# Optimization experiments

Hardware: AMD Instinct MI355X
Metric: run time of the kernel (lower is better)

Reference implementation:

```python
import jax, jax.numpy as jnp
import numpy as np

B, T, N, D, TXT, TE, H = 8, 8192, 256, 512, 768, 2048, 8
DH = D // H


def _ln(x, g, b):
    m = jnp.mean(x, axis=-1, keepdims=True)
    v = jnp.mean(jnp.square(x - m), axis=-1, keepdims=True)
    return (x - m) * jax.lax.rsqrt(v + 1e-5) * g + b


def setup_inputs() -> dict:
    key = jax.random.key(0)
    ks = jax.random.split(key, 10)
    s = 0.02  # init scale for weights (zero_module init replaced by small random for a non-trivial baseline)
    return {
        "x": jax.random.normal(ks[0], (B, T, D), jnp.float32),
        "xf": jax.random.normal(ks[1], (B, N, TXT), jnp.float32),
        "emb": jax.random.normal(ks[2], (B, TE), jnp.float32),
        "ln_x_g": jnp.ones((D,), jnp.float32),
        "ln_x_b": jnp.zeros((D,), jnp.float32),
        "ln_t_g": jnp.ones((TXT,), jnp.float32),
        "ln_t_b": jnp.zeros((TXT,), jnp.float32),
        "Wq": jax.random.normal(ks[3], (D, D), jnp.float32) * s,
        "bq": jnp.zeros((D,), jnp.float32),
        "Wk": jax.random.normal(ks[4], (TXT, D), jnp.float32) * s,
        "bk": jnp.zeros((D,), jnp.float32),
        "Wv": jax.random.normal(ks[5], (TXT, D), jnp.float32) * s,
        "bv": jnp.zeros((D,), jnp.float32),
        "emb_W": jax.random.normal(ks[6], (TE, 2 * D), jnp.float32) * s,
        "emb_b": jnp.zeros((2 * D,), jnp.float32),
        "ln_o_g": jnp.ones((D,), jnp.float32),
        "ln_o_b": jnp.zeros((D,), jnp.float32),
        "out_W": jax.random.normal(ks[7], (D, D), jnp.float32) * s,
        "out_b": jnp.zeros((D,), jnp.float32),
    }


def reference(x, xf, emb, ln_x_g, ln_x_b, ln_t_g, ln_t_b, Wq, bq, Wk, bk, Wv, bv,
              emb_W, emb_b, ln_o_g, ln_o_b, out_W, out_b):
    xt = _ln(xf, ln_t_g, ln_t_b)                                  # [B,N,TXT]
    q = jax.nn.softmax((_ln(x, ln_x_g, ln_x_b) @ Wq + bq).reshape(B, T, H, DH), axis=-1)
    k = jax.nn.softmax((xt @ Wk + bk).reshape(B, N, H, DH), axis=-1)
    v = (xt @ Wv + bv).reshape(B, N, H, DH)
    attn = jnp.einsum('bnhd,bnhl->bhdl', k, v)                    # [B,H,DH,DH] kv aggregation
    out = jnp.einsum('bthd,bhdl->bthl', q, attn).reshape(B, T, D)  # [B,T,D]
    # StylizationBlock
    eo = (jax.nn.silu(emb) @ emb_W + emb_b)[:, None, :]           # [B,1,2D]
    scale, shift = jnp.split(eo, 2, axis=2)
    h = _ln(out, ln_o_g, ln_o_b) * (1 + scale) + shift
    h = jax.nn.silu(h) @ out_W + out_b
    return x + h
```

## Files before the change

### kernel.cpp

```cpp
#include <hip/hip_runtime.h>
#include <hip/hip_bf16.h>
#include <math.h>

#define Bc 8
#define Tc 8192
#define NTOK 256
#define Dc 512
#define TXT 768
#define TEc 2048
#define Hc 8
#define DHc 64
#define MROWS (Bc * Tc)

typedef __attribute__((ext_vector_type(8))) short bf16x8v;
typedef __attribute__((ext_vector_type(8))) unsigned short u16x8;
typedef __attribute__((ext_vector_type(4))) unsigned short u16x4;
typedef __attribute__((ext_vector_type(4))) float f32x4;

#define MFMA16(a, b, c) __builtin_amdgcn_mfma_f32_16x16x32_bf16(a, b, c, 0, 0, 0)

__device__ __forceinline__ unsigned short f2bf(float f) {
    __hip_bfloat16 h = __float2bfloat16(f);
    return __builtin_bit_cast(unsigned short, h);
}
__device__ __forceinline__ float bf2f(unsigned short u) {
    unsigned int x = ((unsigned int)u) << 16;
    return __builtin_bit_cast(float, x);
}

typedef __attribute__((address_space(3))) unsigned int lds_u32_t;
typedef __attribute__((address_space(1))) const unsigned int gbl_u32_t;
__device__ __forceinline__ void gload16(const unsigned short* g, short* l) {
    __builtin_amdgcn_global_load_lds((gbl_u32_t*)g, (lds_u32_t*)l, 16, 0, 0);
}

__device__ __forceinline__ float warp32_reduce_sum(float v) {
    v += __shfl_xor(v, 16); v += __shfl_xor(v, 8); v += __shfl_xor(v, 4);
    v += __shfl_xor(v, 2);  v += __shfl_xor(v, 1);
    return v;
}

__device__ __forceinline__ void transpose_tile(const float* __restrict__ src,
                                               unsigned short* __restrict__ dst,
                                               int N, int rs, int k0, int n0) {
    __shared__ float tile[64][65];
    int tx = threadIdx.x & 63, tq = threadIdx.x >> 6;
#pragma unroll
    for (int i = 0; i < 16; ++i) {
        int kk = tq + i * 4;
        tile[kk][tx] = src[(size_t)(k0 + kk) * N + n0 + tx];
    }
    __syncthreads();
#pragma unroll
    for (int i = 0; i < 16; ++i) {
        int nn = tq + i * 4;
        dst[(size_t)(n0 + nn) * rs + k0 + tx] = f2bf(tile[tx][nn]);
    }
}

__global__ void __launch_bounds__(256) prep_kernel(
    const float* __restrict__ Wq, const float* __restrict__ oW,
    const float* __restrict__ Wk, const float* __restrict__ Wv,
    const float* __restrict__ xf, const float* __restrict__ ln_t_g,
    const float* __restrict__ ln_t_b,
    unsigned short* __restrict__ Wqt, unsigned short* __restrict__ oWt,
    unsigned short* __restrict__ Wkvt, unsigned short* __restrict__ xt) {
    int bid = blockIdx.x;
    if (bid < 64) {
        transpose_tile(Wq, Wqt, Dc, Dc, (bid >> 3) * 64, (bid & 7) * 64);
        return;
    }
    if (bid < 128) {
        int i = bid - 64;
        transpose_tile(oW, oWt, Dc, Dc, (i >> 3) * 64, (i & 7) * 64);
        return;
    }
    if (bid < 224) {
        int i = bid - 128;
        transpose_tile(Wk, Wkvt, Dc, TXT, (i >> 3) * 64, (i & 7) * 64);
        return;
    }
    if (bid < 320) {
        int i = bid - 224;
        transpose_tile(Wv, Wkvt + (size_t)512 * TXT, Dc, TXT, (i >> 3) * 64, (i & 7) * 64);
        return;
    }
    int w = threadIdx.x >> 6, l = threadIdx.x & 63;
    int row = (bid - 320) * 4 + w;
    const float* src = xf + (size_t)row * TXT;
    float4 a0 = *(const float4*)&src[l * 12];
    float4 a1 = *(const float4*)&src[l * 12 + 4];
    float4 a2 = *(const float4*)&src[l * 12 + 8];
    float vals[12] = {a0.x, a0.y, a0.z, a0.w, a1.x, a1.y, a1.z, a1.w,
                      a2.x, a2.y, a2.z, a2.w};
    float s = 0.f, ss = 0.f;
#pragma unroll
    for (int j = 0; j < 12; ++j) { s += vals[j]; ss += vals[j] * vals[j]; }
#pragma unroll
    for (int m = 1; m <= 32; m <<= 1) { s += __shfl_xor(s, m); ss += __shfl_xor(ss, m); }
    float mean = s * (1.f / TXT), var = ss * (1.f / TXT) - mean * mean;
    float rs = rsqrtf(var + 1e-5f);
    unsigned short o[12];
#pragma unroll
    for (int j = 0; j < 12; ++j) {
        int c = l * 12 + j;
        o[j] = f2bf((vals[j] - mean) * rs * ln_t_g[c] + ln_t_b[c]);
    }
    unsigned short* dp = xt + (size_t)row * TXT + l * 12;
    *(u16x4*)&dp[0] = *(u16x4*)&o[0];
    *(u16x4*)&dp[4] = *(u16x4*)&o[4];
    *(u16x4*)&dp[8] = *(u16x4*)&o[8];
}

__global__ void __launch_bounds__(256) ln_x_kernel(const float* __restrict__ x,
                                                   const float* __restrict__ g,
                                                   const float* __restrict__ bt,
                                                   unsigned short* __restrict__ A1) {
    int w = threadIdx.x >> 6, l = threadIdx.x & 63;
    int row = blockIdx.x * 4 + w;
    const float* src = x + (size_t)row * Dc;
    float4 a0 = *(const float4*)&src[l * 8];
    float4 a1 = *(const float4*)&src[l * 8 + 4];
    float vals[8] = {a0.x, a0.y, a0.z, a0.w, a1.x, a1.y, a1.z, a1.w};
    float s = 0.f, ss = 0.f;
#pragma unroll
    for (int j = 0; j < 8; ++j) { s += vals[j]; ss += vals[j] * vals[j]; }
#pragma unroll
    for (int m = 1; m <= 32; m <<= 1) { s += __shfl_xor(s, m); ss += __shfl_xor(ss, m); }
    float mean = s * (1.f / Dc), var = ss * (1.f / Dc) - mean * mean;
    float rs = rsqrtf(var + 1e-5f);
    u16x8 o;
#pragma unroll
    for (int j = 0; j < 8; ++j) {
        int c = l * 8 + j;
        o[j] = f2bf((vals[j] - mean) * rs * g[c] + bt[c]);
    }
    *(u16x8*)&A1[(size_t)row * Dc + l * 8] = o;
}

__global__ void __launch_bounds__(256) kvgemm_kernel(
    const unsigned short* __restrict__ xt, const unsigned short* __restrict__ Wkvt,
    const float* __restrict__ bk, const float* __restrict__ bv,
    unsigned short* __restrict__ kbuf, unsigned short* __restrict__ vbuf) {
    __shared__ short lds_s[16384];
    short* Alds = lds_s;
    short* Blds = lds_s + 8192;

    const int tid = threadIdx.x, l = tid & 63, w = tid >> 6;
    const int lr = l & 15, lg = l >> 4;
    int mt = blockIdx.x >> 3, nt = blockIdx.x & 7;
    int row0 = mt * 128, col0 = nt * 128;
    int wrow = (w >> 1) * 64, wcol = (w & 1) * 64;

    f32x4 acc[4][4] = {};
    const int cbase = w * 64 + l;

    for (int ks = 0; ks < 12; ++ks) {
#pragma unroll
        for (int i = 0; i < 4; ++i) {
            int c = i * 256 + cbase;
            int r = c >> 3, kc = c & 7;
            int koff = ks * 64 + ((kc ^ (r & 7)) << 3);
            gload16(xt + (size_t)(row0 + r) * TXT + koff, &Alds[((i * 4 + w) * 64) * 8]);
            gload16(Wkvt + (size_t)(col0 + r) * TXT + koff, &Blds[((i * 4 + w) * 64) * 8]);
        }
        __syncthreads();
#pragma unroll
        for (int kk = 0; kk < 2; ++kk) {
            int kcw = kk * 4 + lg;
            bf16x8v af[4], bfr[4];
#pragma unroll
            for (int i = 0; i < 4; ++i) {
                int r = wrow + i * 16 + lr;
                af[i] = *(bf16x8v*)&Alds[(r * 8 + (kcw ^ (r & 7))) * 8];
            }
#pragma unroll
            for (int j = 0; j < 4; ++j) {
                int n = wcol + j * 16 + lr;
                bfr[j] = *(bf16x8v*)&Blds[(n * 8 + (kcw ^ (n & 7))) * 8];
            }
#pragma unroll
            for (int i = 0; i < 4; ++i)
#pragma unroll
                for (int j = 0; j < 4; ++j)
                    acc[i][j] = MFMA16(af[i], bfr[j], acc[i][j]);
        }
        __syncthreads();
    }

    const bool kHalf = (col0 + wcol) < 512;
    int cj[4];
    float bias[4];
#pragma unroll
    for (int j = 0; j < 4; ++j) {
        cj[j] = col0 + wcol + j * 16 + lr;
        bias[j] = kHalf ? bk[cj[j]] : bv[cj[j] - 512];
    }
#pragma unroll
    for (int i = 0; i < 4; ++i)
#pragma unroll
        for (int reg = 0; reg < 4; ++reg) {
            float v0 = acc[i][0][reg] + bias[0], v1 = acc[i][1][reg] + bias[1];
            float v2 = acc[i][2][reg] + bias[2], v3 = acc[i][3][reg] + bias[3];
            if (kHalf) {
                float m = fmaxf(fmaxf(v0, v1), fmaxf(v2, v3));
                m = fmaxf(m, __shfl_xor(m, 1)); m = fmaxf(m, __shfl_xor(m, 2));
                m = fmaxf(m, __shfl_xor(m, 4)); m = fmaxf(m, __shfl_xor(m, 8));
                float e0 = __expf(v0 - m), e1 = __expf(v1 - m);
                float e2 = __expf(v2 - m), e3 = __expf(v3 - m);
                float ssum = e0 + e1 + e2 + e3;
                ssum += __shfl_xor(ssum, 1); ssum += __shfl_xor(ssum, 2);
                ssum += __shfl_xor(ssum, 4); ssum += __shfl_xor(ssum, 8);
                float inv = 1.f / ssum;
                v0 = e0 * inv; v1 = e1 * inv; v2 = e2 * inv; v3 = e3 * inv;
            }
            int r = row0 + wrow + i * 16 + 4 * lg + reg;
            float vv[4] = {v0, v1, v2, v3};
#pragma unroll
            for (int j = 0; j < 4; ++j) {
                if (kHalf) kbuf[(size_t)r * Dc + cj[j]] = f2bf(vv[j]);
                else       vbuf[(size_t)r * Dc + cj[j] - 512] = f2bf(vv[j]);
            }
        }
}

__global__ void __launch_bounds__(512) attn_kernel(const unsigned short* __restrict__ kbuf,
                                                   const unsigned short* __restrict__ vbuf,
                                                   unsigned short* __restrict__ attn_t) {
    __shared__ unsigned short ksh[128][DHc], vsh[128][DHc];
    const int tid = threadIdx.x;
    const int b = blockIdx.x >> 3, h = blockIdx.x & 7;
    const int d = tid >> 3, lb = (tid & 7) * 8;
    const int tok = tid >> 2, c0 = (tid & 3) * 16;
    float acc[8] = {0.f};
    for (int st = 0; st < 2; ++st) {
        __syncthreads();
        size_t o = (size_t)(b * NTOK + st * 128 + tok) * Dc + h * DHc + c0;
        *(u16x8*)&ksh[tok][c0]     = *(const u16x8*)&kbuf[o];
        *(u16x8*)&ksh[tok][c0 + 8] = *(const u16x8*)&kbuf[o + 8];
        *(u16x8*)&vsh[tok][c0]     = *(const u16x8*)&vbuf[o];
        *(u16x8*)&vsh[tok][c0 + 8] = *(const u16x8*)&vbuf[o + 8];
        __syncthreads();
        for (int n = 0; n < 128; ++n) {
            float kd = bf2f(ksh[n][d]);
            u16x4 va = *(const u16x4*)&vsh[n][lb];
            u16x4 vb = *(const u16x4*)&vsh[n][lb + 4];
#pragma unroll
            for (int e = 0; e < 4; ++e) acc[e] += kd * bf2f(va[e]);
#pragma unroll
            for (int e = 0; e < 4; ++e) acc[4 + e] += kd * bf2f(vb[e]);
        }
    }
    size_t base = (size_t)(b * 8 + h) * DHc * DHc;
#pragma unroll
    for (int e = 0; e < 8; ++e)
        attn_t[base + (size_t)(lb + e) * DHc + d] = f2bf(acc[e]);
}

__global__ void __launch_bounds__(256) emb_kernel(const float* __restrict__ emb,
                                                  const float* __restrict__ emb_W,
                                                  const float* __restrict__ emb_b,
                                                  float* __restrict__ eo) {
    __shared__ float s[4][TEc];
    __shared__ float red[4][64][4];
    const int tid = threadIdx.x;
    const int chunk = blockIdx.x >> 1, bh = blockIdx.x & 1;
#pragma unroll
    for (int j = 0; j < 8; ++j) {
        int idx = tid + 256 * j;
        int bi = idx >> 9, kk4 = (idx & 511) * 4;
#pragma unroll
        for (int e = 0; e < 4; ++e) {
            float v = emb[(bh * 4 + bi) * TEc + kk4 + e];
            s[bi][kk4 + e] = v / (1.f + __expf(-v));
        }
    }
    __syncthreads();
    int c = tid & 63, q = tid >> 6;
    int col = chunk * 64 + c;
    float acc[4] = {0.f, 0.f, 0.f, 0.f};
    for (int kk = q * 512; kk < q * 512 + 512; ++kk) {
        float wv = emb_W[(size_t)kk * (2 * Dc) + col];
#pragma unroll
        for (int bi = 0; bi < 4; ++bi) acc[bi] += s[bi][kk] * wv;
    }
#pragma unroll
    for (int bi = 0; bi < 4; ++bi) red[q][c][bi] = acc[bi];
    __syncthreads();
    if (q == 0) {
        float bb = emb_b[col];
#pragma unroll
        for (int bi = 0; bi < 4; ++bi)
            eo[(bh * 4 + bi) * (2 * Dc) + col] =
                red[0][c][bi] + red[1][c][bi] + red[2][c][bi] + red[3][c][bi] + bb;
    }
}

__global__ void __launch_bounds__(512, 4) gemm1_kernel(
    const unsigned short* __restrict__ A1, const unsigned short* __restrict__ Wt,
    const float* __restrict__ bq, const unsigned short* __restrict__ attn_t,
    unsigned short* __restrict__ out1) {
    __shared__ short lds_s[24576];
    short* Alds = lds_s;
    short* Blds = lds_s + 16384;

    const int tid = threadIdx.x, l = tid & 63, w = tid >> 6;
    const int lr = l & 15, lg = l >> 4;
    int raw = blockIdx.x;
    int swz = (raw & 7) * 128 + (raw >> 3);
    int mt = swz >> 2, nt = swz & 3;
    int row0 = mt * 256, col0 = nt * 128;
    int b = row0 >> 13;
    int wrow = (w >> 1) * 64, wcol = (w & 1) * 64;

    f32x4 acc[4][4] = {};

    for (int ks = 0; ks < 8; ++ks) {
#pragma unroll
        for (int i = 0; i < 4; ++i) {
            int c = i * 512 + tid;
            int r = c >> 3, kc = c & 7;
            int koff = ks * 64 + ((kc ^ (r & 7)) << 3);
            gload16(A1 + (size_t)(row0 + r) * Dc + koff, &Alds[(i * 8 + w) * 512]);
        }
#pragma unroll
        for (int i = 0; i < 2; ++i) {
            int c = i * 512 + tid;
            int r = c >> 3, kc = c & 7;
            int koff = ks * 64 + ((kc ^ (r & 7)) << 3);
            gload16(Wt + (size_t)(col0 + r) * Dc + koff, &Blds[(i * 8 + w) * 512]);
        }
        __syncthreads();
#pragma unroll
        for (int kk = 0; kk < 2; ++kk) {
            int kcw = kk * 4 + lg;
            bf16x8v af[4], bfr[4];
#pragma unroll
            for (int i = 0; i < 4; ++i) {
                int r = wrow + i * 16 + lr;
                af[i] = *(bf16x8v*)&Alds[(r * 8 + (kcw ^ (r & 7))) * 8];
            }
#pragma unroll
            for (int j = 0; j < 4; ++j) {
                int n = wcol + j * 16 + lr;
                bfr[j] = *(bf16x8v*)&Blds[(n * 8 + (kcw ^ (n & 7))) * 8];
            }
#pragma unroll
            for (int i = 0; i < 4; ++i)
#pragma unroll
                for (int j = 0; j < 4; ++j)
                    acc[i][j] = MFMA16(af[i], bfr[j], acc[i][j]);
        }
        __syncthreads();
    }

    float bqv[4];
#pragma unroll
    for (int j = 0; j < 4; ++j) bqv[j] = bq[col0 + wcol + j * 16 + lr];

    int hw = nt * 2 + (w & 1);
    const unsigned short* at = attn_t + (size_t)(b * 8 + hw) * DHc * DHc;
    short* Qw = lds_s + w * 1024;

#pragma unroll
    for (int i = 0; i < 4; ++i) {
#pragma unroll
        for (int reg = 0; reg < 4; ++reg) {
            float v0 = acc[i][0][reg] + bqv[0], v1 = acc[i][1][reg] + bqv[1];
            float v2 = acc[i][2][reg] + bqv[2], v3 = acc[i][3][reg] + bqv[3];
            float m = fmaxf(fmaxf(v0, v1), fmaxf(v2, v3));
            m = fmaxf(m, __shfl_xor(m, 1)); m = fmaxf(m, __shfl_xor(m, 2));
            m = fmaxf(m, __shfl_xor(m, 4)); m = fmaxf(m, __shfl_xor(m, 8));
            float e0 = __expf(v0 - m), e1 = __expf(v1 - m);
            float e2 = __expf(v2 - m), e3 = __expf(v3 - m);
            float ssum = e0 + e1 + e2 + e3;
            ssum += __shfl_xor(ssum, 1); ssum += __shfl_xor(ssum, 2);
            ssum += __shfl_xor(ssum, 4); ssum += __shfl_xor(ssum, 8);
            float inv = 1.f / ssum;
            acc[i][0][reg] = e0 * inv; acc[i][1][reg] = e1 * inv;
            acc[i][2][reg] = e2 * inv; acc[i][3][reg] = e3 * inv;
        }
#pragma unroll
        for (int j = 0; j < 4; ++j)
#pragma unroll
            for (int reg = 0; reg < 4; ++reg) {
                int rl = 4 * lg + reg;
                int c = j * 16 + lr;
                Qw[(rl * 8 + ((c >> 3) ^ (rl & 7))) * 8 + (c & 7)] =
                    (short)f2bf(acc[i][j][reg]);
            }
        f32x4 acc2[4] = {};
#pragma unroll
        for (int kk = 0; kk < 2; ++kk) {
            int kc = kk * 4 + lg;
            bf16x8v a = *(bf16x8v*)&Qw[(lr * 8 + (kc ^ (lr & 7))) * 8];
            bf16x8v bf2[4];
#pragma unroll
            for (int j = 0; j < 4; ++j)
                bf2[j] = *(const bf16x8v*)&at[(j * 16 + lr) * DHc + kk * 32 + lg * 8];
#pragma unroll
            for (int j = 0; j < 4; ++j)
                acc2[j] = MFMA16(a, bf2[j], acc2[j]);
        }
#pragma unroll
        for (int j = 0; j < 4; ++j)
#pragma unroll
            for (int reg = 0; reg < 4; ++reg) {
                int r = row0 + wrow + i * 16 + 4 * lg + reg;
                int c = col0 + wcol + j * 16 + lr;
                out1[(size_t)r * Dc + c] = f2bf(acc2[j][reg]);
            }
    }
}

__global__ void __launch_bounds__(256) mid_kernel(const unsigned short* __restrict__ out1,
                                                  const float* __restrict__ eo,
                                                  const float* __restrict__ g,
                                                  const float* __restrict__ bt,
                                                  unsigned short* __restrict__ A2) {
    int w = threadIdx.x >> 6, l = threadIdx.x & 63;
    int row = blockIdx.x * 4 + w;
    int b = row >> 13;
    u16x8 iv = *(const u16x8*)&out1[(size_t)row * Dc + l * 8];
    float vals[8];
    float s = 0.f, ss = 0.f;
#pragma unroll
    for (int j = 0; j < 8; ++j) {
        vals[j] = bf2f(iv[j]);
        s += vals[j]; ss += vals[j] * vals[j];
    }
#pragma unroll
    for (int m = 1; m <= 32; m <<= 1) { s += __shfl_xor(s, m); ss += __shfl_xor(ss, m); }
    float mean = s * (1.f / Dc), var = ss * (1.f / Dc) - mean * mean;
    float rs = rsqrtf(var + 1e-5f);
    const float* scl = eo + (size_t)b * (2 * Dc);
    const float* shf = scl + Dc;
    u16x8 o;
#pragma unroll
    for (int j = 0; j < 8; ++j) {
        int c = l * 8 + j;
        float t = (vals[j] - mean) * rs * g[c] + bt[c];
        t = t * (1.f + scl[c]) + shf[c];
        t = t / (1.f + __expf(-t));
        o[j] = f2bf(t);
    }
    *(u16x8*)&A2[(size_t)row * Dc + l * 8] = o;
}

__global__ void __launch_bounds__(512, 4) gemm2_kernel(
    const unsigned short* __restrict__ A2, const unsigned short* __restrict__ Wt,
    const float* __restrict__ ob, const float* __restrict__ x,
    float* __restrict__ out) {
    __shared__ short lds_s[24576];
    short* Alds = lds_s;
    short* Blds = lds_s + 16384;

    const int tid = threadIdx.x, l = tid & 63, w = tid >> 6;
    const int lr = l & 15, lg = l >> 4;
    int raw = blockIdx.x;
    int swz = (raw & 7) * 128 + (raw >> 3);
    int mt = swz >> 2, nt = swz & 3;
    int row0 = mt * 256, col0 = nt * 128;
    int wrow = (w >> 1) * 64, wcol = (w & 1) * 64;

    f32x4 acc[4][4] = {};

    for (int ks = 0; ks < 8; ++ks) {
#pragma unroll
        for (int i = 0; i < 4; ++i) {
            int c = i * 512 + tid;
            int r = c >> 3, kc = c & 7;
            int koff = ks * 64 + ((kc ^ (r & 7)) << 3);
            gload16(A2 + (size_t)(row0 + r) * Dc + koff, &Alds[(i * 8 + w) * 512]);
        }
#pragma unroll
        for (int i = 0; i < 2; ++i) {
            int c = i * 512 + tid;
            int r = c >> 3, kc = c & 7;
            int koff = ks * 64 + ((kc ^ (r & 7)) << 3);
            gload16(Wt + (size_t)(col0 + r) * Dc + koff, &Blds[(i * 8 + w) * 512]);
        }
        __syncthreads();
#pragma unroll
        for (int kk = 0; kk < 2; ++kk) {
            int kcw = kk * 4 + lg;
            bf16x8v af[4], bfr[4];
#pragma unroll
            for (int i = 0; i < 4; ++i) {
                int r = wrow + i * 16 + lr;
                af[i] = *(bf16x8v*)&Alds[(r * 8 + (kcw ^ (r & 7))) * 8];
            }
#pragma unroll
            for (int j = 0; j < 4; ++j) {
                int n = wcol + j * 16 + lr;
                bfr[j] = *(bf16x8v*)&Blds[(n * 8 + (kcw ^ (n & 7))) * 8];
            }
#pragma unroll
            for (int i = 0; i < 4; ++i)
#pragma unroll
                for (int j = 0; j < 4; ++j)
                    acc[i][j] = MFMA16(af[i], bfr[j], acc[i][j]);
        }
        __syncthreads();
    }

    float obv[4];
#pragma unroll
    for (int j = 0; j < 4; ++j) obv[j] = ob[col0 + wcol + j * 16 + lr];
#pragma unroll
    for (int i = 0; i < 4; ++i)
#pragma unroll
        for (int j = 0; j < 4; ++j)
#pragma unroll
            for (int reg = 0; reg < 4; ++reg) {
                int r = row0 + wrow + i * 16 + 4 * lg + reg;
                int c = col0 + wcol + j * 16 + lr;
                size_t o = (size_t)r * Dc + c;
                out[o] = acc[i][j][reg] + obv[j] + x[o];
            }
}

extern "C" void kernel_launch(void* const* d_in, const int* in_sizes, int n_in,
                              void* d_out, int out_size, void* d_ws, size_t ws_size,
                              hipStream_t stream) {
    const float* x      = (const float*)d_in[0];
    const float* xf     = (const float*)d_in[1];
    const float* emb    = (const float*)d_in[2];
    const float* ln_x_g = (const float*)d_in[3];
    const float* ln_x_b = (const float*)d_in[4];
    const float* ln_t_g = (const float*)d_in[5];
    const float* ln_t_b = (const float*)d_in[6];
    const float* Wq     = (const float*)d_in[7];
    const float* bq     = (const float*)d_in[8];
    const float* Wk     = (const float*)d_in[9];
    const float* bk     = (const float*)d_in[10];
    const float* Wv     = (const float*)d_in[11];
    const float* bv     = (const float*)d_in[12];
    const float* emb_W  = (const float*)d_in[13];
    const float* emb_b  = (const float*)d_in[14];
    const float* ln_o_g = (const float*)d_in[15];
    const float* ln_o_b = (const float*)d_in[16];
    const float* out_W  = (const float*)d_in[17];
    const float* out_b  = (const float*)d_in[18];
    float* out = (float*)d_out;

    unsigned short* xt   = (unsigned short*)d_ws;
    unsigned short* kbuf = xt + (size_t)2048 * TXT;
    unsigned short* vbuf = kbuf + (size_t)2048 * 512;
    unsigned short* Wkvt = vbuf + (size_t)2048 * 512;
    unsigned short* Wqt  = Wkvt + (size_t)1024 * TXT;
    unsigned short* oWt  = Wqt + (size_t)512 * 512;
    unsigned short* attn_t = oWt + (size_t)512 * 512;
    float* eo = (float*)(attn_t + (size_t)64 * 64 * 64);
    unsigned short* out1 = (unsigned short*)(eo + 8 * 1024);
    unsigned short* A1   = out1 + (size_t)MROWS * Dc;
    unsigned short* A2   = A1;

    hipLaunchKernelGGL(prep_kernel, dim3(832), dim3(256), 0, stream,
                       Wq, out_W, Wk, Wv, xf, ln_t_g, ln_t_b, Wqt, oWt, Wkvt, xt);
    hipLaunchKernelGGL(ln_x_kernel, dim3(MROWS / 4), dim3(256), 0, stream,
                       x, ln_x_g, ln_x_b, A1);
    hipLaunchKernelGGL(kvgemm_kernel, dim3(16 * 8), dim3(256), 0, stream,
                       xt, Wkvt, bk, bv, kbuf, vbuf);
    hipLaunchKernelGGL(attn_kernel, dim3(Bc * Hc), dim3(512), 0, stream,
                       kbuf, vbuf, attn_t);
    hipLaunchKernelGGL(emb_kernel, dim3(32), dim3(256), 0, stream, emb, emb_W, emb_b, eo);
    hipLaunchKernelGGL(gemm1_kernel, dim3(MROWS / 256 * 4), dim3(512), 0, stream,
                       A1, Wqt, bq, attn_t, out1);
    hipLaunchKernelGGL(mid_kernel, dim3(MROWS / 4), dim3(256), 0, stream,
                       out1, eo, ln_o_g, ln_o_b, A2);
    hipLaunchKernelGGL(gemm2_kernel, dim3(MROWS / 256 * 4), dim3(512), 0, stream,
                       A2, oWt, out_b, x, out);
}
```

Measured before the change: 298.5 us.

## Prefetch residual x in gemm2, widen emb grid, share prep LDS buffer

gemm2 now issues volatile loads of the residual x tile during its last four k-steps so the data is warm in cache before the epilogue reads it. emb_kernel is restructured to one batch per block with 128 blocks instead of 32 blocks that each handle four batches, which raises parallelism at the cost of reading emb_W more times. The transpose tile in prep_kernel now uses a shared LDS buffer passed in as a parameter, and gemm1's head index is rewritten in terms of wcol. The dummy loads add VMEM traffic and register use inside the main gemm2 loop.

```diff
diff --git a/kernel.cpp b/kernel.cpp
--- a/kernel.cpp
+++ b/kernel.cpp
@@ -34,16 +34,11 @@
     __builtin_amdgcn_global_load_lds((gbl_u32_t*)g, (lds_u32_t*)l, 16, 0, 0);
 }
 
-__device__ __forceinline__ float warp32_reduce_sum(float v) {
-    v += __shfl_xor(v, 16); v += __shfl_xor(v, 8); v += __shfl_xor(v, 4);
-    v += __shfl_xor(v, 2);  v += __shfl_xor(v, 1);
-    return v;
-}
-
 __device__ __forceinline__ void transpose_tile(const float* __restrict__ src,
                                                unsigned short* __restrict__ dst,
-                                               int N, int rs, int k0, int n0) {
-    __shared__ float tile[64][65];
+                                               int N, int rs, int k0, int n0,
+                                               char* smem) {
+    float (*tile)[65] = (float(*)[65])smem;
     int tx = threadIdx.x & 63, tq = threadIdx.x >> 6;
 #pragma unroll
     for (int i = 0; i < 16; ++i) {
@@ -65,24 +60,25 @@
     const float* __restrict__ ln_t_b,
     unsigned short* __restrict__ Wqt, unsigned short* __restrict__ oWt,
     unsigned short* __restrict__ Wkvt, unsigned short* __restrict__ xt) {
+    __shared__ __align__(16) char smem[16704];
     int bid = blockIdx.x;
     if (bid < 64) {
-        transpose_tile(Wq, Wqt, Dc, Dc, (bid >> 3) * 64, (bid & 7) * 64);
+        transpose_tile(Wq, Wqt, Dc, Dc, (bid >> 3) * 64, (bid & 7) * 64, smem);
         return;
     }
     if (bid < 128) {
         int i = bid - 64;
-        transpose_tile(oW, oWt, Dc, Dc, (i >> 3) * 64, (i & 7) * 64);
+        transpose_tile(oW, oWt, Dc, Dc, (i >> 3) * 64, (i & 7) * 64, smem);
         return;
     }
     if (bid < 224) {
         int i = bid - 128;
-        transpose_tile(Wk, Wkvt, Dc, TXT, (i >> 3) * 64, (i & 7) * 64);
+        transpose_tile(Wk, Wkvt, Dc, TXT, (i >> 3) * 64, (i & 7) * 64, smem);
         return;
     }
     if (bid < 320) {
         int i = bid - 224;
-        transpose_tile(Wv, Wkvt + (size_t)512 * TXT, Dc, TXT, (i >> 3) * 64, (i & 7) * 64);
+        transpose_tile(Wv, Wkvt + (size_t)512 * TXT, Dc, TXT, (i >> 3) * 64, (i & 7) * 64, smem);
         return;
     }
     int w = threadIdx.x >> 6, l = threadIdx.x & 63;
@@ -110,6 +106,32 @@
     *(u16x4*)&dp[0] = *(u16x4*)&o[0];
     *(u16x4*)&dp[4] = *(u16x4*)&o[4];
     *(u16x4*)&dp[8] = *(u16x4*)&o[8];
+}
+
+__global__ void __launch_bounds__(256) emb_kernel(const float* __restrict__ emb,
+                                                  const float* __restrict__ emb_W,
+                                                  const float* __restrict__ emb_b,
+                                                  float* __restrict__ eo) {
+    __shared__ float s[TEc];
+    __shared__ float red[4][64];
+    const int tid = threadIdx.x;
+    const int b = blockIdx.x >> 4, chunk = blockIdx.x & 15;
+#pragma unroll
+    for (int j = 0; j < 8; ++j) {
+        int idx = tid + 256 * j;
+        float e = emb[b * TEc + idx];
+        s[idx] = e / (1.f + __expf(-e));
+    }
+    __syncthreads();
+    int c = tid & 63, q = tid >> 6;
+    int col = chunk * 64 + c;
+    float acc = 0.f;
+    for (int kk = q * 512; kk < q * 512 + 512; ++kk)
+        acc += s[kk] * emb_W[(size_t)kk * (2 * Dc) + col];
+    red[q][c] = acc;
+    __syncthreads();
+    if (q == 0)
+        eo[b * (2 * Dc) + col] = red[0][c] + red[1][c] + red[2][c] + red[3][c] + emb_b[col];
 }
 
 __global__ void __launch_bounds__(256) ln_x_kernel(const float* __restrict__ x,
@@ -257,45 +279,6 @@
         attn_t[base + (size_t)(lb + e) * DHc + d] = f2bf(acc[e]);
 }
 
-__global__ void __launch_bounds__(256) emb_kernel(const float* __restrict__ emb,
-                                                  const float* __restrict__ emb_W,
-                                                  const float* __restrict__ emb_b,
-                                                  float* __restrict__ eo) {
-    __shared__ float s[4][TEc];
-    __shared__ float red[4][64][4];
-    const int tid = threadIdx.x;
-    const int chunk = blockIdx.x >> 1, bh = blockIdx.x & 1;
-#pragma unroll
-    for (int j = 0; j < 8; ++j) {
-        int idx = tid + 256 * j;
-        int bi = idx >> 9, kk4 = (idx & 511) * 4;
-#pragma unroll
-        for (int e = 0; e < 4; ++e) {
-            float v = emb[(bh * 4 + bi) * TEc + kk4 + e];
-            s[bi][kk4 + e] = v / (1.f + __expf(-v));
-        }
-    }
-    __syncthreads();
-    int c = tid & 63, q = tid >> 6;
-    int col = chunk * 64 + c;
-    float acc[4] = {0.f, 0.f, 0.f, 0.f};
-    for (int kk = q * 512; kk < q * 512 + 512; ++kk) {
-        float wv = emb_W[(size_t)kk * (2 * Dc) + col];
-#pragma unroll
-        for (int bi = 0; bi < 4; ++bi) acc[bi] += s[bi][kk] * wv;
-    }
-#pragma unroll
-    for (int bi = 0; bi < 4; ++bi) red[q][c][bi] = acc[bi];
-    __syncthreads();
-    if (q == 0) {
-        float bb = emb_b[col];
-#pragma unroll
-        for (int bi = 0; bi < 4; ++bi)
-            eo[(bh * 4 + bi) * (2 * Dc) + col] =
-                red[0][c][bi] + red[1][c][bi] + red[2][c][bi] + red[3][c][bi] + bb;
-    }
-}
-
 __global__ void __launch_bounds__(512, 4) gemm1_kernel(
     const unsigned short* __restrict__ A1, const unsigned short* __restrict__ Wt,
     const float* __restrict__ bq, const unsigned short* __restrict__ attn_t,
@@ -358,7 +341,7 @@
 #pragma unroll
     for (int j = 0; j < 4; ++j) bqv[j] = bq[col0 + wcol + j * 16 + lr];
 
-    int hw = nt * 2 + (w & 1);
+    int hw = nt * 2 + (wcol >> 6);
     const unsigned short* at = attn_t + (size_t)(b * 8 + hw) * DHc * DHc;
     short* Qw = lds_s + w * 1024;
 
@@ -464,6 +447,7 @@
     int wrow = (w >> 1) * 64, wcol = (w & 1) * 64;
 
     f32x4 acc[4][4] = {};
+    const volatile float* xv = x;
 
     for (int ks = 0; ks < 8; ++ks) {
 #pragma unroll
@@ -479,6 +463,17 @@
             int r = c >> 3, kc = c & 7;
             int koff = ks * 64 + ((kc ^ (r & 7)) << 3);
             gload16(Wt + (size_t)(col0 + r) * Dc + koff, &Blds[(i * 8 + w) * 512]);
+        }
+        if (ks >= 4) {
+            int i = ks - 4;
+            size_t xbase = (size_t)(row0 + wrow + i * 16 + 4 * lg) * Dc + col0 + wcol + lr;
+#pragma unroll
+            for (int reg = 0; reg < 4; ++reg)
+#pragma unroll
+                for (int j = 0; j < 4; ++j) {
+                    float t = xv[xbase + (size_t)reg * Dc + j * 16];
+                    asm volatile("" :: "v"(t));
+                }
         }
         __syncthreads();
 #pragma unroll
@@ -564,7 +559,8 @@
                        xt, Wkvt, bk, bv, kbuf, vbuf);
     hipLaunchKernelGGL(attn_kernel, dim3(Bc * Hc), dim3(512), 0, stream,
                        kbuf, vbuf, attn_t);
-    hipLaunchKernelGGL(emb_kernel, dim3(32), dim3(256), 0, stream, emb, emb_W, emb_b, eo);
+    hipLaunchKernelGGL(emb_kernel, dim3(Bc * 16), dim3(256), 0, stream,
+                       emb, emb_W, emb_b, eo);
     hipLaunchKernelGGL(gemm1_kernel, dim3(MROWS / 256 * 4), dim3(512), 0, stream,
                        A1, Wqt, bq, attn_t, out1);
     hipLaunchKernelGGL(mid_kernel, dim3(MROWS / 4), dim3(256), 0, stream,
```

Result: slower. 342.0 us (+14.6%).
